# Kernel optimization log

Measured on AMD Instinct MI355X. Metric: run time of the kernel, lower is better.

Reference implementation:

```python
import jax, jax.numpy as jnp
import numpy as np

B, N, NG = 32, 64, 100   # batch, atoms, gaussians in srdf
NB, NF, MAXZ = 128, 256, 20  # n_basis, n_factors, max atomic number
N_INTERACTIONS = 3


def setup_inputs() -> dict:
    key = jax.random.key(0)
    ks = jax.random.split(key, 12)
    r = np.sqrt(1.0 / np.sqrt(float(NB))).astype(np.float32)
    return {
        "Z": jax.random.randint(ks[0], (B, N), 0, MAXZ, dtype=jnp.int32),
        "C": jax.random.uniform(ks[1], (B, N, N, NG), dtype=jnp.float32),
        # learned parameters
        "W_emb": jax.random.normal(ks[2], (MAXZ, NB), dtype=jnp.float32) * r,
        "Wc": jax.random.normal(ks[3], (NG, NF), dtype=jnp.float32) * 0.1,
        "bc": jnp.zeros((NF,), dtype=jnp.float32),
        "Wi": jax.random.normal(ks[4], (NB, NF), dtype=jnp.float32) * 0.1,  # in2fac (shared across passes)
        "bi": jnp.zeros((NF,), dtype=jnp.float32),
        "Wf": jax.random.normal(ks[5], (NF, NB), dtype=jnp.float32) * 0.1,  # fac2out (shared)
        "W1": jax.random.normal(ks[6], (NB, NB // 2), dtype=jnp.float32) * 0.1,
        "b1": jnp.zeros((NB // 2,), dtype=jnp.float32),
        "W2": jax.random.normal(ks[7], (NB // 2, 1), dtype=jnp.float32) * 0.1,
        "b2": jnp.zeros((1,), dtype=jnp.float32),
    }


def reference(Z, C, W_emb, Wc, bc, Wi, bi, Wf, W1, b1, W2, b2):
    # pairwise mask: valid atom pairs (Z_i>0 and Z_j>0), diagonal removed
    pair = Z[:, :, None] * Z[:, None, :]                      # [B,N,N]
    offdiag = 1.0 - jnp.eye(N, dtype=jnp.float32)
    mask = (pair > 0).astype(jnp.float32) * offdiag           # [B,N,N]
    mask = mask[..., None]                                    # [B,N,N,1]

    # atom embedding via one-hot lookup == row gather
    X = W_emb[Z]                                              # [B,N,NB]
    # distance basis -> factor space
    fC = jnp.einsum('bijg,gf->bijf', C, Wc) + bc              # [B,N,N,NF]

    for _ in range(N_INTERACTIONS):
        fX = X @ Wi + bi                                      # [B,N,NF]
        fVj = fX[:, None, :, :] * fC                          # [B,N,N,NF]
        Vj = jnp.tanh(jnp.einsum('bijf,fo->bijo', fVj, Wf))   # [B,N,N,NB]
        V = jnp.sum(Vj * mask, axis=2)                        # masked sum over neighbors j
        X = X + V

    o1 = jnp.tanh(X @ W1 + b1)                                # [B,N,NB//2]
    yi = o1 @ W2 + b2                                         # [B,N,1]; std=1, mu=0 -> identity
    atom_mask = (Z > 0).astype(jnp.float32)[..., None]        # [B,N,1]
    y = jnp.sum(yi * atom_mask, axis=1)                       # [B,1] total energy
    return y
```

## Files before the change

### kernel.cpp

```cpp
#include <hip/hip_runtime.h>
#include <hip/hip_bf16.h>
#include <math.h>

#define BB   32
#define NN   64
#define NGG  100
#define NBB  128
#define NFF  256
#define NITER 3
#define KPAD 128

typedef _Float16 f16x8 __attribute__((ext_vector_type(8)));
typedef _Float16 f16x4 __attribute__((ext_vector_type(4)));
typedef float    f32x4 __attribute__((ext_vector_type(4)));

static __device__ __forceinline__ float fast_exp2(float x) {
    float r; asm("v_exp_f32 %0, %1" : "=v"(r) : "v"(x)); return r;
}
static __device__ __forceinline__ float fast_rcp(float x) {
    float r; asm("v_rcp_f32 %0, %1" : "=v"(r) : "v"(x)); return r;
}
static __device__ __forceinline__ float fast_tanh(float x) {
    float p = fast_exp2(x * 2.8853900817779268f);
    return 1.0f - 2.0f * fast_rcp(p + 1.0f);
}

#define EMB_N (BB * NN * NBB)
#define WCF_N (NFF * KPAD)
#define WFF_N (NBB * NFF)
#define WIF_N (NBB * NFF)
#define W1F_N (NBB * 64)
#define PREP_TOTAL (EMB_N + WCF_N + WFF_N + WIF_N + W1F_N)
#define PREP_GRID (PREP_TOTAL / 256)
__global__ void prep_kernel(const int* __restrict__ Z, const float* __restrict__ W_emb,
                            const float* __restrict__ Wc, const float* __restrict__ Wf,
                            const float* __restrict__ Wi, const float* __restrict__ W1,
                            float* __restrict__ X, _Float16* __restrict__ WcF,
                            _Float16* __restrict__ WfF, _Float16* __restrict__ WiF,
                            _Float16* __restrict__ W1F) {
    int idx = blockIdx.x * 256 + threadIdx.x;
    if (idx < EMB_N) {
        int bn = idx >> 7, t = idx & 127;
        X[idx] = W_emb[Z[bn] * NBB + t];
        return;
    }
    idx -= EMB_N;
    if (idx < WCF_N) {
        int e = idx & 7, lane = (idx >> 3) & 63, ks = (idx >> 9) & 3, ct = (idx >> 11) & 3, w = idx >> 13;
        int l15 = lane & 15, kg = lane >> 4;
        int f = w * 64 + ct * 16 + l15;
        int k = ks * 32 + kg * 8 + e;
        WcF[idx] = (k < NGG) ? (_Float16)Wc[(size_t)k * NFF + f] : (_Float16)0.f;
        return;
    }
    idx -= WCF_N;
    if (idx < WFF_N) {
        int e = idx & 7, lane = (idx >> 3) & 63, ks = (idx >> 9) & 7, ct = (idx >> 12) & 1, w = idx >> 13;
        int l15 = lane & 15, kg = lane >> 4;
        int o = w * 32 + ct * 16 + l15;
        int k = ks * 32 + kg * 8 + e;
        WfF[idx] = (_Float16)Wf[(size_t)k * NBB + o];
        return;
    }
    idx -= WFF_N;
    if (idx < WIF_N) {
        int e = idx & 7, lane = (idx >> 3) & 63, ks = (idx >> 9) & 3, ct16 = idx >> 11;
        int l15 = lane & 15, kg = lane >> 4;
        int f = ct16 * 16 + l15;
        int k = ks * 32 + kg * 8 + e;
        WiF[idx] = (_Float16)Wi[(size_t)k * NFF + f];
        return;
    }
    idx -= WIF_N;
    if (idx < W1F_N) {
        int e = idx & 7, lane = (idx >> 3) & 63, ks = (idx >> 9) & 3, ct16 = idx >> 11;
        int l15 = lane & 15, kg = lane >> 4;
        int o = ct16 * 16 + l15;
        int k = ks * 32 + kg * 8 + e;
        W1F[idx] = (_Float16)W1[(size_t)k * 64 + o];
    }
}

__global__ void transpose_pad_kernel(const float* __restrict__ src, _Float16* __restrict__ dst,
                                     int K, int Kpad, int NC) {
    int idx = blockIdx.x * 256 + threadIdx.x;
    if (idx >= NC * Kpad) return;
    int c = idx / Kpad, k = idx - c * Kpad;
    dst[idx] = (k < K) ? (_Float16)src[(size_t)k * NC + c] : (_Float16)0.f;
}

static __device__ __forceinline__ void stage_C(const float* Crow_base, _Float16* Cs, int t) {
    const int r = t >> 2, q = t & 3;
    const float* Crow = Crow_base + (size_t)r * NGG;
    const int sw = (r & 7) << 3;
    #pragma unroll
    for (int m = 0; m < 8; ++m) {
        const int k = q * 32 + m * 4;
        f16x4 h = {0.f, 0.f, 0.f, 0.f};
        if (k < NGG) {
            float4 v = *(const float4*)(Crow + k);
            h[0] = (_Float16)v.x; h[1] = (_Float16)v.y;
            h[2] = (_Float16)v.z; h[3] = (_Float16)v.w;
        }
        *(f16x4*)&Cs[r * KPAD + (k ^ sw)] = h;
    }
}
static __device__ __forceinline__ void stage_X(const float* Xrow_base, _Float16* Xs, int t) {
    const int r = t >> 2, q = t & 3;
    const float* Xrow = Xrow_base + (size_t)r * NBB;
    const int sw = (r & 7) << 3;
    #pragma unroll
    for (int m = 0; m < 8; ++m) {
        const int k = q * 32 + m * 4;
        float4 v = *(const float4*)(Xrow + k);
        f16x4 h;
        h[0] = (_Float16)v.x; h[1] = (_Float16)v.y;
        h[2] = (_Float16)v.z; h[3] = (_Float16)v.w;
        *(f16x4*)&Xs[r * KPAD + (k ^ sw)] = h;
    }
}

static __device__ __forceinline__ void fc_body(
    int bi_, int t, _Float16* Cs,
    const int* __restrict__ Z, const float* __restrict__ C,
    const _Float16* __restrict__ WcF, const float* __restrict__ bc,
    _Float16* __restrict__ fCF)
{
    const int b = bi_ >> 6, i = bi_ & 63;
    if (Z[b * NN + i] == 0) return;

    const int wave = t >> 6, lane = t & 63;
    const int l15 = lane & 15, kg = lane >> 4;

    stage_C(C + (size_t)bi_ * NN * NGG, Cs, t);

    f16x8 aw[4][4];
    float4 bcq[4];
    #pragma unroll
    for (int ct = 0; ct < 4; ++ct) {
        #pragma unroll
        for (int ks = 0; ks < 4; ++ks)
            aw[ct][ks] = *(const f16x8*)&WcF[(size_t)(((wave * 4 + ct) * 4 + ks) * 64 + lane) * 8];
        bcq[ct] = *(const float4*)&bc[wave * 64 + ct * 16 + kg * 4];
    }
    __syncthreads();

    #pragma unroll
    for (int jt = 0; jt < 4; ++jt) {
        const int j = jt * 16 + l15;
        const int sw = (l15 & 7) << 3;
        f16x8 bfr[4];
        #pragma unroll
        for (int ks = 0; ks < 4; ++ks)
            bfr[ks] = *(const f16x8*)&Cs[j * KPAD + ((ks * 32 + kg * 8) ^ sw)];
        #pragma unroll
        for (int ct = 0; ct < 4; ++ct) {
            f32x4 acc = {bcq[ct].x, bcq[ct].y, bcq[ct].z, bcq[ct].w};
            #pragma unroll
            for (int ks = 0; ks < 4; ++ks)
                acc = __builtin_amdgcn_mfma_f32_16x16x32_f16(aw[ct][ks], bfr[ks], acc, 0, 0, 0);
            const int u = ct * 16 + kg * 4;
            const int ksf = wave * 2 + (u >> 5);
            const int kgf = (u >> 3) & 3;
            const int e0 = u & 4;
            f16x4 o;
            o[0] = (_Float16)acc[0]; o[1] = (_Float16)acc[1];
            o[2] = (_Float16)acc[2]; o[3] = (_Float16)acc[3];
            size_t off = ((size_t)(bi_ * 32 + jt * 8 + ksf) * 64 + (kgf * 16 + l15)) * 8 + e0;
            *(f16x4*)&fCF[off] = o;
        }
    }
}

static __device__ __forceinline__ void fxm_body(
    int b, int fq, int t, _Float16* Xs,
    const float* __restrict__ X, const _Float16* __restrict__ WiF,
    const float* __restrict__ bi, const int* __restrict__ Z,
    _Float16* __restrict__ fXF)
{
    const int wave = t >> 6, lane = t & 63;
    const int l15 = lane & 15, kg = lane >> 4;
    const int ct16 = fq * 4 + wave;

    stage_X(X + (size_t)b * NN * NBB, Xs, t);

    f16x8 aw[4];
    #pragma unroll
    for (int ks = 0; ks < 4; ++ks)
        aw[ks] = *(const f16x8*)&WiF[(size_t)((ct16 * 4 + ks) * 64 + lane) * 8];
    float4 biq = *(const float4*)&bi[ct16 * 16 + kg * 4];
    __syncthreads();

    f32x4 acc[4];
    #pragma unroll
    for (int jt = 0; jt < 4; ++jt) acc[jt] = (f32x4){biq.x, biq.y, biq.z, biq.w};

    #pragma unroll
    for (int ks = 0; ks < 4; ++ks) {
        #pragma unroll
        for (int jt = 0; jt < 4; ++jt) {
            const int j = jt * 16 + l15;
            const int sw = (l15 & 7) << 3;
            f16x8 bfr = *(const f16x8*)&Xs[j * KPAD + ((ks * 32 + kg * 8) ^ sw)];
            acc[jt] = __builtin_amdgcn_mfma_f32_16x16x32_f16(aw[ks], bfr, acc[jt], 0, 0, 0);
        }
    }

    const int u_g = ct16 * 16 + kg * 4;
    const int ks_t = u_g >> 5, kg_t = (u_g >> 3) & 3, e0 = u_g & 4;
    #pragma unroll
    for (int jt = 0; jt < 4; ++jt) {
        const int j = jt * 16 + l15;
        const int zj = Z[b * NN + j];
        f16x4 o = {0.f, 0.f, 0.f, 0.f};
        if (zj > 0) {
            o[0] = (_Float16)acc[jt][0]; o[1] = (_Float16)acc[jt][1];
            o[2] = (_Float16)acc[jt][2]; o[3] = (_Float16)acc[jt][3];
        }
        size_t off = ((size_t)(b * 32 + jt * 8 + ks_t) * 64 + (kg_t * 16 + l15)) * 8 + e0;
        *(f16x4*)&fXF[off] = o;
    }
}

#define FXM_GRID (BB * 4)

__global__ __launch_bounds__(256) void fxm_kernel(
    const float* __restrict__ X, const _Float16* __restrict__ WiF,
    const float* __restrict__ bi, const int* __restrict__ Z,
    _Float16* __restrict__ fXF)
{
    __shared__ __align__(16) _Float16 Xs[NN * KPAD];
    fxm_body(blockIdx.x >> 2, blockIdx.x & 3, threadIdx.x, Xs, X, WiF, bi, Z, fXF);
}

__global__ __launch_bounds__(256, 3) void fcfx_kernel(
    const int* __restrict__ Z, const float* __restrict__ C,
    const _Float16* __restrict__ WcF, const float* __restrict__ bc,
    _Float16* __restrict__ fCF,
    const float* __restrict__ X, const _Float16* __restrict__ WiF,
    const float* __restrict__ bi, _Float16* __restrict__ fXF)
{
    __shared__ __align__(16) _Float16 S[NN * KPAD];
    if (blockIdx.x < FXM_GRID)
        fxm_body(blockIdx.x >> 2, blockIdx.x & 3, threadIdx.x, S, X, WiF, bi, Z, fXF);
    else
        fc_body(blockIdx.x - FXM_GRID, threadIdx.x, S, Z, C, WcF, bc, fCF);
}

__global__ __launch_bounds__(256) void interact_lite(
    const int* __restrict__ Z, const _Float16* __restrict__ fCF,
    const _Float16* __restrict__ WfF, const _Float16* __restrict__ fXF,
    float* __restrict__ X)
{
    const int bi_ = blockIdx.x;
    const int b = bi_ >> 6, i = bi_ & 63;
    if (Z[b * NN + i] == 0) return;

    const int t = threadIdx.x;
    const int wave = t >> 6, lane = t & 63;
    const int kg = lane >> 4;

    f16x8 bwf[2][8];
    #pragma unroll
    for (int ct = 0; ct < 2; ++ct)
        #pragma unroll
        for (int ks = 0; ks < 8; ++ks)
            bwf[ct][ks] = *(const f16x8*)&WfF[(size_t)(((wave * 2 + ct) * 8 + ks) * 64 + lane) * 8];

    const size_t cbase = (size_t)bi_ * 32;
    const size_t xbase = (size_t)b * 32;

    f32x4 a[4][2];
    #pragma unroll
    for (int jt = 0; jt < 4; ++jt) {
        a[jt][0] = (f32x4){0.f, 0.f, 0.f, 0.f};
        a[jt][1] = (f32x4){0.f, 0.f, 0.f, 0.f};
    }

    #pragma unroll
    for (int ks = 0; ks < 8; ++ks) {
        #pragma unroll
        for (int jt = 0; jt < 4; ++jt) {
            f16x8 fc = *(const f16x8*)&fCF[((cbase + jt * 8 + ks) * 64 + lane) * 8];
            f16x8 fx = *(const f16x8*)&fXF[((xbase + jt * 8 + ks) * 64 + lane) * 8];
            f16x8 av = fc * fx;
            a[jt][0] = __builtin_amdgcn_mfma_f32_16x16x32_f16(av, bwf[0][ks], a[jt][0], 0, 0, 0);
            a[jt][1] = __builtin_amdgcn_mfma_f32_16x16x32_f16(av, bwf[1][ks], a[jt][1], 0, 0, 0);
        }
    }

    float vsum0 = 0.f, vsum1 = 0.f;
    #pragma unroll
    for (int jt = 0; jt < 4; ++jt) {
        #pragma unroll
        for (int reg = 0; reg < 4; ++reg) {
            int j2 = jt * 16 + kg * 4 + reg;
            if (j2 != i) {
                vsum0 += fast_tanh(a[jt][0][reg]);
                vsum1 += fast_tanh(a[jt][1][reg]);
            }
        }
    }
    vsum0 += __shfl_xor(vsum0, 16); vsum0 += __shfl_xor(vsum0, 32);
    vsum1 += __shfl_xor(vsum1, 16); vsum1 += __shfl_xor(vsum1, 32);
    if (lane < 16) {
        float* Xp = X + (size_t)bi_ * NBB + wave * 32 + lane;
        Xp[0]  += vsum0;
        Xp[16] += vsum1;
    }
}

__global__ __launch_bounds__(256, 3) void interact_fused(
    const int* __restrict__ Z, const float* __restrict__ C,
    const _Float16* __restrict__ WcT, const float* __restrict__ bc,
    const _Float16* __restrict__ WfT, const _Float16* __restrict__ fXF,
    float* __restrict__ X)
{
    __shared__ __align__(16) _Float16 Cs[NN * KPAD];
    __shared__ __align__(16) _Float16 fVs[NN * NFF];

    const int bi_ = blockIdx.x;
    const int b = bi_ >> 6, i = bi_ & 63;
    if (Z[b * NN + i] == 0) return;

    const int t = threadIdx.x;
    const int wave = t >> 6, lane = t & 63;
    const int l15 = lane & 15, kg = lane >> 4;

    stage_C(C + (size_t)bi_ * NN * NGG, Cs, t);

    f16x8 aw[4][4];
    float4 bcq[4];
    #pragma unroll
    for (int ct = 0; ct < 4; ++ct) {
        #pragma unroll
        for (int ks = 0; ks < 4; ++ks)
            aw[ct][ks] = *(const f16x8*)&WcT[(size_t)(wave * 64 + ct * 16 + l15) * KPAD + ks * 32 + kg * 8];
        bcq[ct] = *(const float4*)&bc[wave * 64 + ct * 16 + kg * 4];
    }
    __syncthreads();

    #pragma unroll
    for (int jt = 0; jt < 4; ++jt) {
        const int j = jt * 16 + l15;
        const int sw = (l15 & 7) << 3;
        f16x8 bfr[4];
        #pragma unroll
        for (int ks = 0; ks < 4; ++ks)
            bfr[ks] = *(const f16x8*)&Cs[j * KPAD + ((ks * 32 + kg * 8) ^ sw)];
        #pragma unroll
        for (int ct = 0; ct < 4; ++ct) {
            f32x4 acc = {bcq[ct].x, bcq[ct].y, bcq[ct].z, bcq[ct].w};
            #pragma unroll
            for (int ks = 0; ks < 4; ++ks)
                acc = __builtin_amdgcn_mfma_f32_16x16x32_f16(aw[ct][ks], bfr[ks], acc, 0, 0, 0);
            const int u = ct * 16 + kg * 4;
            const int ksf = wave * 2 + (u >> 5);
            const int kgf = (u >> 3) & 3;
            const int e0 = u & 4;
            f16x4 fx4 = *(const f16x4*)&fXF[((size_t)(b * 32 + jt * 8 + ksf) * 64 + (kgf * 16 + l15)) * 8 + e0];
            const int f0 = wave * 64 + u;
            f16x4 o;
            o[0] = (_Float16)(acc[0] * (float)fx4[0]);
            o[1] = (_Float16)(acc[1] * (float)fx4[1]);
            o[2] = (_Float16)(acc[2] * (float)fx4[2]);
            o[3] = (_Float16)(acc[3] * (float)fx4[3]);
            *(f16x4*)&fVs[j * NFF + (f0 ^ ((j & 7) << 3))] = o;
        }
    }
    __syncthreads();

    f16x8 bwf[2][8];
    #pragma unroll
    for (int ct = 0; ct < 2; ++ct)
        #pragma unroll
        for (int ks = 0; ks < 8; ++ks)
            bwf[ct][ks] = *(const f16x8*)&WfT[(size_t)(wave * 32 + ct * 16 + l15) * NFF + ks * 32 + kg * 8];

    float vsum0 = 0.f, vsum1 = 0.f;
    #pragma unroll
    for (int jt = 0; jt < 4; ++jt) {
        const int r = jt * 16 + l15;
        const int sw = (l15 & 7) << 3;
        f32x4 a0 = {0.f, 0.f, 0.f, 0.f}, a1 = {0.f, 0.f, 0.f, 0.f};
        #pragma unroll
        for (int ks = 0; ks < 8; ++ks) {
            f16x8 av = *(const f16x8*)&fVs[r * NFF + ((ks * 32 + kg * 8) ^ sw)];
            a0 = __builtin_amdgcn_mfma_f32_16x16x32_f16(av, bwf[0][ks], a0, 0, 0, 0);
            a1 = __builtin_amdgcn_mfma_f32_16x16x32_f16(av, bwf[1][ks], a1, 0, 0, 0);
        }
        #pragma unroll
        for (int reg = 0; reg < 4; ++reg) {
            int j2 = jt * 16 + kg * 4 + reg;
            if (j2 != i) {
                vsum0 += fast_tanh(a0[reg]);
                vsum1 += fast_tanh(a1[reg]);
            }
        }
    }
    vsum0 += __shfl_xor(vsum0, 16); vsum0 += __shfl_xor(vsum0, 32);
    vsum1 += __shfl_xor(vsum1, 16); vsum1 += __shfl_xor(vsum1, 32);
    if (lane < 16) {
        float* Xp = X + (size_t)bi_ * NBB + wave * 32 + lane;
        Xp[0]  += vsum0;
        Xp[16] += vsum1;
    }
}

__global__ __launch_bounds__(256) void readout_kernel(
    const int* __restrict__ Z, const float* __restrict__ X,
    const _Float16* __restrict__ W1F, const float* __restrict__ b1,
    const float* __restrict__ W2, const float* __restrict__ b2,
    float* __restrict__ y)
{
    __shared__ __align__(16) _Float16 Xs[NN * KPAD];
    __shared__ float part[4][NN];
    const int b = blockIdx.x, t = threadIdx.x;
    const int wave = t >> 6, lane = t & 63;
    const int l15 = lane & 15, kg = lane >> 4;

    stage_X(X + (size_t)b * NN * NBB, Xs, t);

    f16x8 aw[4];
    #pragma unroll
    for (int ks = 0; ks < 4; ++ks)
        aw[ks] = *(const f16x8*)&W1F[(size_t)((wave * 4 + ks) * 64 + lane) * 8];
    float4 b1q = *(const float4*)&b1[wave * 16 + kg * 4];
    float4 w2q = *(const float4*)&W2[wave * 16 + kg * 4];
    __syncthreads();

    f32x4 acc[4];
    #pragma unroll
    for (int jt = 0; jt < 4; ++jt) acc[jt] = (f32x4){b1q.x, b1q.y, b1q.z, b1q.w};

    #pragma unroll
    for (int ks = 0; ks < 4; ++ks) {
        #pragma unroll
        for (int jt = 0; jt < 4; ++jt) {
            const int j = jt * 16 + l15;
            const int sw = (l15 & 7) << 3;
            f16x8 bfr = *(const f16x8*)&Xs[j * KPAD + ((ks * 32 + kg * 8) ^ sw)];
            acc[jt] = __builtin_amdgcn_mfma_f32_16x16x32_f16(aw[ks], bfr, acc[jt], 0, 0, 0);
        }
    }

    #pragma unroll
    for (int jt = 0; jt < 4; ++jt) {
        float s = fast_tanh(acc[jt][0]) * w2q.x + fast_tanh(acc[jt][1]) * w2q.y
                + fast_tanh(acc[jt][2]) * w2q.z + fast_tanh(acc[jt][3]) * w2q.w;
        s += __shfl_xor(s, 16); s += __shfl_xor(s, 32);
        if (lane < 16) part[wave][jt * 16 + lane] = s;
    }
    __syncthreads();

    if (t < NN) {
        float s = part[0][t] + part[1][t] + part[2][t] + part[3][t] + b2[0];
        float v = (Z[b * NN + t] > 0) ? s : 0.f;
        #pragma unroll
        for (int off = 32; off > 0; off >>= 1) v += __shfl_down(v, off);
        if (t == 0) y[b] = v;
    }
}

extern "C" void kernel_launch(void* const* d_in, const int* in_sizes, int n_in,
                              void* d_out, int out_size, void* d_ws, size_t ws_size,
                              hipStream_t stream) {
    (void)in_sizes; (void)n_in; (void)out_size;
    const int*   Z    = (const int*)d_in[0];
    const float* C    = (const float*)d_in[1];
    const float* Wemb = (const float*)d_in[2];
    const float* Wc   = (const float*)d_in[3];
    const float* bc   = (const float*)d_in[4];
    const float* Wi   = (const float*)d_in[5];
    const float* bi   = (const float*)d_in[6];
    const float* Wf   = (const float*)d_in[7];
    const float* W1   = (const float*)d_in[8];
    const float* b1   = (const float*)d_in[9];
    const float* W2   = (const float*)d_in[10];
    const float* b2   = (const float*)d_in[11];
    float* y = (float*)d_out;

    char* p = (char*)d_ws;
    float*    X   = (float*)p;      p += (size_t)BB * NN * NBB * 4;
    _Float16* fXF = (_Float16*)p;   p += (size_t)BB * NN * NFF * 2;
    _Float16* WcF = (_Float16*)p;   p += (size_t)WCF_N * 2;
    _Float16* WfF = (_Float16*)p;   p += (size_t)WFF_N * 2;
    _Float16* WiF = (_Float16*)p;   p += (size_t)WIF_N * 2;
    _Float16* W1F = (_Float16*)p;   p += (size_t)W1F_N * 2;
    _Float16* WcT = (_Float16*)p;   p += (size_t)NFF * KPAD * 2;
    _Float16* WfT = (_Float16*)p;   p += (size_t)NBB * NFF * 2;
    size_t base = (size_t)(p - (char*)d_ws);
    size_t fcf_bytes = (size_t)BB * NN * NN * NFF * 2;
    bool split = (ws_size >= base + fcf_bytes);
    _Float16* fCF = (_Float16*)p;

    prep_kernel<<<PREP_GRID, 256, 0, stream>>>(Z, Wemb, Wc, Wf, Wi, W1, X, WcF, WfF, WiF, W1F);

    if (split) {
        fcfx_kernel<<<FXM_GRID + BB * NN, 256, 0, stream>>>(Z, C, WcF, bc, fCF, X, WiF, bi, fXF);
        interact_lite<<<BB * NN, 256, 0, stream>>>(Z, fCF, WfF, fXF, X);
        for (int it = 1; it < NITER; ++it) {
            fxm_kernel<<<FXM_GRID, 256, 0, stream>>>(X, WiF, bi, Z, fXF);
            interact_lite<<<BB * NN, 256, 0, stream>>>(Z, fCF, WfF, fXF, X);
        }
    } else {
        transpose_pad_kernel<<<(NFF * KPAD) / 256, 256, 0, stream>>>(Wc, WcT, NGG, KPAD, NFF);
        transpose_pad_kernel<<<(NBB * NFF) / 256, 256, 0, stream>>>(Wf, WfT, NFF, NFF, NBB);
        for (int it = 0; it < NITER; ++it) {
            fxm_kernel<<<FXM_GRID, 256, 0, stream>>>(X, WiF, bi, Z, fXF);
            interact_fused<<<BB * NN, 256, 0, stream>>>(Z, C, WcT, bc, WfT, fXF, X);
        }
    }
    readout_kernel<<<BB, 256, 0, stream>>>(Z, X, W1F, b1, W2, b2, y);
}
```

Baseline: 124.9 us.

## Fuse next-iteration fX projection into interaction kernel tail with ping-pong buffers

```diff
diff --git a/kernel.cpp b/kernel.cpp
--- a/kernel.cpp
+++ b/kernel.cpp
@@ -176,7 +176,7 @@
     int b, int fq, int t, _Float16* Xs,
     const float* __restrict__ X, const _Float16* __restrict__ WiF,
     const float* __restrict__ bi, const int* __restrict__ Z,
-    _Float16* __restrict__ fXF)
+    _Float16* __restrict__ fXF, _Float16* __restrict__ fXFz)
 {
     const int wave = t >> 6, lane = t & 63;
     const int l15 = lane & 15, kg = lane >> 4;
@@ -213,11 +213,13 @@
         const int j = jt * 16 + l15;
         const int zj = Z[b * NN + j];
         f16x4 o = {0.f, 0.f, 0.f, 0.f};
+        size_t off = ((size_t)(b * 32 + jt * 8 + ks_t) * 64 + (kg_t * 16 + l15)) * 8 + e0;
         if (zj > 0) {
             o[0] = (_Float16)acc[jt][0]; o[1] = (_Float16)acc[jt][1];
             o[2] = (_Float16)acc[jt][2]; o[3] = (_Float16)acc[jt][3];
-        }
-        size_t off = ((size_t)(b * 32 + jt * 8 + ks_t) * 64 + (kg_t * 16 + l15)) * 8 + e0;
+        } else {
+            *(f16x4*)&fXFz[off] = o;
+        }
         *(f16x4*)&fXF[off] = o;
     }
 }
@@ -230,7 +232,7 @@
     _Float16* __restrict__ fXF)
 {
     __shared__ __align__(16) _Float16 Xs[NN * KPAD];
-    fxm_body(blockIdx.x >> 2, blockIdx.x & 3, threadIdx.x, Xs, X, WiF, bi, Z, fXF);
+    fxm_body(blockIdx.x >> 2, blockIdx.x & 3, threadIdx.x, Xs, X, WiF, bi, Z, fXF, fXF);
 }
 
 __global__ __launch_bounds__(256, 3) void fcfx_kernel(
@@ -238,20 +240,25 @@
     const _Float16* __restrict__ WcF, const float* __restrict__ bc,
     _Float16* __restrict__ fCF,
     const float* __restrict__ X, const _Float16* __restrict__ WiF,
-    const float* __restrict__ bi, _Float16* __restrict__ fXF)
+    const float* __restrict__ bi, _Float16* __restrict__ fXF,
+    _Float16* __restrict__ fXFz)
 {
     __shared__ __align__(16) _Float16 S[NN * KPAD];
     if (blockIdx.x < FXM_GRID)
-        fxm_body(blockIdx.x >> 2, blockIdx.x & 3, threadIdx.x, S, X, WiF, bi, Z, fXF);
+        fxm_body(blockIdx.x >> 2, blockIdx.x & 3, threadIdx.x, S, X, WiF, bi, Z, fXF, fXFz);
     else
         fc_body(blockIdx.x - FXM_GRID, threadIdx.x, S, Z, C, WcF, bc, fCF);
 }
 
+template<int TAIL>
 __global__ __launch_bounds__(256) void interact_lite(
     const int* __restrict__ Z, const _Float16* __restrict__ fCF,
-    const _Float16* __restrict__ WfF, const _Float16* __restrict__ fXF,
-    float* __restrict__ X)
-{
+    const _Float16* __restrict__ WfF, const _Float16* __restrict__ fXin,
+    _Float16* __restrict__ fXout,
+    float* __restrict__ X, const float* __restrict__ Wi,
+    const float* __restrict__ bi)
+{
+    __shared__ float xrow[NBB];
     const int bi_ = blockIdx.x;
     const int b = bi_ >> 6, i = bi_ & 63;
     if (Z[b * NN + i] == 0) return;
@@ -282,7 +289,7 @@
         #pragma unroll
         for (int jt = 0; jt < 4; ++jt) {
             f16x8 fc = *(const f16x8*)&fCF[((cbase + jt * 8 + ks) * 64 + lane) * 8];
-            f16x8 fx = *(const f16x8*)&fXF[((xbase + jt * 8 + ks) * 64 + lane) * 8];
+            f16x8 fx = *(const f16x8*)&fXin[((xbase + jt * 8 + ks) * 64 + lane) * 8];
             f16x8 av = fc * fx;
             a[jt][0] = __builtin_amdgcn_mfma_f32_16x16x32_f16(av, bwf[0][ks], a[jt][0], 0, 0, 0);
             a[jt][1] = __builtin_amdgcn_mfma_f32_16x16x32_f16(av, bwf[1][ks], a[jt][1], 0, 0, 0);
@@ -305,8 +312,28 @@
     vsum1 += __shfl_xor(vsum1, 16); vsum1 += __shfl_xor(vsum1, 32);
     if (lane < 16) {
         float* Xp = X + (size_t)bi_ * NBB + wave * 32 + lane;
-        Xp[0]  += vsum0;
-        Xp[16] += vsum1;
+        float n0 = Xp[0]  + vsum0;
+        float n1 = Xp[16] + vsum1;
+        Xp[0]  = n0;
+        Xp[16] = n1;
+        if (TAIL) {
+            xrow[wave * 32 + lane]      = n0;
+            xrow[wave * 32 + lane + 16] = n1;
+        }
+    }
+
+    if (TAIL) {
+        __syncthreads();
+        float acc0 = bi[t], acc1 = 0.f;
+        #pragma unroll 8
+        for (int k = 0; k < NBB; k += 2) {
+            acc0 += xrow[k]     * Wi[(size_t)k * NFF + t];
+            acc1 += xrow[k + 1] * Wi[(size_t)(k + 1) * NFF + t];
+        }
+        float acc = acc0 + acc1;
+        const int jt = i >> 4, l15r = i & 15;
+        const int ksx = t >> 5, kg2 = (t >> 3) & 3, e = t & 7;
+        fXout[((size_t)(b * 32 + jt * 8 + ksx) * 64 + (kg2 * 16 + l15r)) * 8 + e] = (_Float16)acc;
     }
 }
 
@@ -481,14 +508,15 @@
     float* y = (float*)d_out;
 
     char* p = (char*)d_ws;
-    float*    X   = (float*)p;      p += (size_t)BB * NN * NBB * 4;
-    _Float16* fXF = (_Float16*)p;   p += (size_t)BB * NN * NFF * 2;
-    _Float16* WcF = (_Float16*)p;   p += (size_t)WCF_N * 2;
-    _Float16* WfF = (_Float16*)p;   p += (size_t)WFF_N * 2;
-    _Float16* WiF = (_Float16*)p;   p += (size_t)WIF_N * 2;
-    _Float16* W1F = (_Float16*)p;   p += (size_t)W1F_N * 2;
-    _Float16* WcT = (_Float16*)p;   p += (size_t)NFF * KPAD * 2;
-    _Float16* WfT = (_Float16*)p;   p += (size_t)NBB * NFF * 2;
+    float*    X    = (float*)p;      p += (size_t)BB * NN * NBB * 4;
+    _Float16* fXFa = (_Float16*)p;   p += (size_t)BB * NN * NFF * 2;
+    _Float16* fXFb = (_Float16*)p;   p += (size_t)BB * NN * NFF * 2;
+    _Float16* WcF  = (_Float16*)p;   p += (size_t)WCF_N * 2;
+    _Float16* WfF  = (_Float16*)p;   p += (size_t)WFF_N * 2;
+    _Float16* WiF  = (_Float16*)p;   p += (size_t)WIF_N * 2;
+    _Float16* W1F  = (_Float16*)p;   p += (size_t)W1F_N * 2;
+    _Float16* WcT  = (_Float16*)p;   p += (size_t)NFF * KPAD * 2;
+    _Float16* WfT  = (_Float16*)p;   p += (size_t)NBB * NFF * 2;
     size_t base = (size_t)(p - (char*)d_ws);
     size_t fcf_bytes = (size_t)BB * NN * NN * NFF * 2;
     bool split = (ws_size >= base + fcf_bytes);
@@ -497,18 +525,16 @@
     prep_kernel<<<PREP_GRID, 256, 0, stream>>>(Z, Wemb, Wc, Wf, Wi, W1, X, WcF, WfF, WiF, W1F);
 
     if (split) {
-        fcfx_kernel<<<FXM_GRID + BB * NN, 256, 0, stream>>>(Z, C, WcF, bc, fCF, X, WiF, bi, fXF);
-        interact_lite<<<BB * NN, 256, 0, stream>>>(Z, fCF, WfF, fXF, X);
-        for (int it = 1; it < NITER; ++it) {
-            fxm_kernel<<<FXM_GRID, 256, 0, stream>>>(X, WiF, bi, Z, fXF);
-            interact_lite<<<BB * NN, 256, 0, stream>>>(Z, fCF, WfF, fXF, X);
-        }
+        fcfx_kernel<<<FXM_GRID + BB * NN, 256, 0, stream>>>(Z, C, WcF, bc, fCF, X, WiF, bi, fXFa, fXFb);
+        interact_lite<1><<<BB * NN, 256, 0, stream>>>(Z, fCF, WfF, fXFa, fXFb, X, Wi, bi);
+        interact_lite<1><<<BB * NN, 256, 0, stream>>>(Z, fCF, WfF, fXFb, fXFa, X, Wi, bi);
+        interact_lite<0><<<BB * NN, 256, 0, stream>>>(Z, fCF, WfF, fXFa, fXFb, X, Wi, bi);
     } else {
         transpose_pad_kernel<<<(NFF * KPAD) / 256, 256, 0, stream>>>(Wc, WcT, NGG, KPAD, NFF);
         transpose_pad_kernel<<<(NBB * NFF) / 256, 256, 0, stream>>>(Wf, WfT, NFF, NFF, NBB);
         for (int it = 0; it < NITER; ++it) {
-            fxm_kernel<<<FXM_GRID, 256, 0, stream>>>(X, WiF, bi, Z, fXF);
-            interact_fused<<<BB * NN, 256, 0, stream>>>(Z, C, WcT, bc, WfT, fXF, X);
+            fxm_kernel<<<FXM_GRID, 256, 0, stream>>>(X, WiF, bi, Z, fXFa);
+            interact_fused<<<BB * NN, 256, 0, stream>>>(Z, C, WcT, bc, WfT, fXFa, X);
         }
     }
     readout_kernel<<<BB, 256, 0, stream>>>(Z, X, W1F, b1, W2, b2, y);
```

Measured after the change: 132.3 us. 5.9% more time.
